# Performance work log

Measured on AMD Instinct MI355X. Metric: run time of the kernel, lower is better.

## Reference

```python
import jax, jax.numpy as jnp
import numpy as np

B, S, D_MODEL, N_HEAD, D_HEAD, GROUPS = 2, 1024, 768, 12, 64, 4
EPS = 1e-9
SCALE = 1.0 / np.sqrt(D_HEAD).astype(np.float32)


def grouped_proj(x, W, b=None):
    # grouped 1x1 Conv1d == block-diagonal linear. x: [B,S,D], W: [g, D/g, O/g]
    g = W.shape[0]
    b_, s_, d = x.shape
    y = jnp.einsum("bsgi,gio->bsgo", x.reshape(b_, s_, g, d // g), W).reshape(b_, s_, -1)
    return y if b is None else y + b


def rel_shift_gather(pos_attn, context_len, shift):
    # HF Funnel _relative_shift_gather
    b, n, s, m = pos_attn.shape
    pos_attn = pos_attn.reshape(b, n, m, s)[:, :, shift:, :]
    pos_attn = pos_attn.reshape(b, n, s, m - shift)[..., :context_len]
    return pos_attn


def setup_inputs() -> dict:
    key = jax.random.key(0)
    ks = jax.random.split(key, 16)
    dg = D_MODEL // GROUPS          # in-channels per group
    og = (N_HEAD * D_HEAD) // GROUPS  # out-channels per group
    std = 0.02
    return {
        "query": jax.random.normal(ks[0], (B, S, D_MODEL), jnp.float32),
        "position_embeds": jax.random.normal(ks[1], (2 * S - 1, D_MODEL), jnp.float32),
        "Wq": jax.random.normal(ks[2], (GROUPS, dg, og), jnp.float32) * std,
        "Wk": jax.random.normal(ks[3], (GROUPS, dg, og), jnp.float32) * std,
        "bk": jnp.zeros((N_HEAD * D_HEAD,), jnp.float32),
        "Wv": jax.random.normal(ks[4], (GROUPS, dg, dg), jnp.float32) * std,
        "bv": jnp.zeros((D_MODEL,), jnp.float32),
        "r_kernel": jax.random.normal(ks[5], (D_MODEL, N_HEAD, D_HEAD), jnp.float32) * std,
        "r_w_bias": jax.random.normal(ks[6], (N_HEAD, D_HEAD), jnp.float32) * std,
        "r_r_bias": jax.random.normal(ks[7], (N_HEAD, D_HEAD), jnp.float32) * std,
        "Wo": jax.random.normal(ks[8], (D_MODEL, D_MODEL), jnp.float32) * std,
        "bo": jnp.zeros((D_MODEL,), jnp.float32),
        "gamma": jnp.ones((D_MODEL,), jnp.float32),
        "beta": jnp.zeros((D_MODEL,), jnp.float32),
    }


def reference(query, position_embeds, Wq, Wk, bk, Wv, bv, r_kernel, r_w_bias,
              r_r_bias, Wo, bo, gamma, beta):
    b, s, _ = query.shape
    # q/k/v via grouped 1x1 convs
    q = grouped_proj(query, Wq).reshape(b, s, N_HEAD, D_HEAD) * SCALE
    k = grouped_proj(query, Wk, bk).reshape(b, s, N_HEAD, D_HEAD)
    v = grouped_proj(query, Wv, bv).reshape(b, s, N_HEAD, D_MODEL // N_HEAD)
    # content stream: (q + u) k^T
    content_score = jnp.einsum("bind,bjnd->bnij", q + r_w_bias * SCALE, k)
    # position stream: (q + v) r^T over 2S-1 relative positions, then rel-shift
    r_head = jnp.einsum("td,dnh->tnh", position_embeds, r_kernel)
    pos_score = jnp.einsum("bind,tnd->bnit", q + r_r_bias * SCALE, r_head)
    pos_score = rel_shift_gather(pos_score, s, shift=1)
    attn_prob = jax.nn.softmax(content_score + pos_score, axis=-1)
    attn_vec = jnp.einsum("bnij,bjnd->bind", attn_prob, v).reshape(b, s, D_MODEL)
    attn_out = attn_vec @ Wo + bo
    # residual + layer norm (eps=1e-9)
    h = query + attn_out
    mu = jnp.mean(h, axis=-1, keepdims=True)
    var = jnp.mean(jnp.square(h - mu), axis=-1, keepdims=True)
    return (h - mu) * jax.lax.rsqrt(var + EPS) * gamma + beta
```

## Files before the change

kernel.cpp:

```cpp
#include <hip/hip_runtime.h>
#include <stdint.h>

#define B_ 2
#define S_ 1024
#define D_ 768
#define H_ 12
#define DH 64
#define G_ 4
#define DG 192
#define T_ 2047
#define SCALEF 0.125f

typedef unsigned short u16;
typedef unsigned int u32;
typedef __attribute__((ext_vector_type(8))) short short8;
typedef __attribute__((ext_vector_type(4))) float floatx4;

__device__ __forceinline__ float uas(u32 x){ union { u32 i; float f; } v; v.i = x; return v.f; }
__device__ __forceinline__ float bf2f(u16 u){ return uas(((u32)u) << 16); }
__device__ __forceinline__ u16 f2bf(float f){
    union { float f; u32 i; } v; v.f = f;
    u32 x = v.i;
    u32 r = (x + 0x7fffu + ((x >> 16) & 1u)) >> 16;
    return (u16)r;
}

__global__ __launch_bounds__(256) void proj_kernel(
    const float* __restrict__ query,
    const float* __restrict__ Wq, const float* __restrict__ Wk, const float* __restrict__ Wv,
    const float* __restrict__ bk, const float* __restrict__ bv,
    u16* __restrict__ qq, u16* __restrict__ ko, u16* __restrict__ vt)
{
    __shared__ u16 As[64][40];
    __shared__ u16 Ws[3][64][38];
    int tid  = threadIdx.x;
    int wave = tid >> 6, lane = tid & 63;
    int qm   = lane & 15;
    int quad = lane >> 4;
    int k8   = quad * 8;
    int m0 = blockIdx.x * 64;
    int g  = blockIdx.y / 3;
    int n0 = (blockIdx.y % 3) * 64;

    const float* Wm[3] = { Wq, Wk, Wv };

    floatx4 acc[3][4];
    #pragma unroll
    for (int md = 0; md < 3; md++)
        #pragma unroll
        for (int bt = 0; bt < 4; bt++) acc[md][bt] = (floatx4){0.f,0.f,0.f,0.f};

    for (int kt = 0; kt < 6; kt++) {
        int k0 = kt * 32;
        #pragma unroll
        for (int p = 0; p < 8; p++) {
            int idx = p*256 + tid;
            int m = idx >> 5, k = idx & 31;
            As[m][k] = f2bf(query[(size_t)(m0 + m)*D_ + g*DG + k0 + k]);
        }
        #pragma unroll
        for (int md = 0; md < 3; md++) {
            const float* W = Wm[md] + (size_t)g*DG*DG;
            #pragma unroll
            for (int p = 0; p < 8; p++) {
                int k = p*4 + (tid >> 6);
                int n = tid & 63;
                Ws[md][n][k] = f2bf(W[(size_t)(k0 + k)*DG + n0 + n]);
            }
        }
        __syncthreads();
        short8 a = *(const short8*)&As[wave*16 + qm][k8];
        #pragma unroll
        for (int md = 0; md < 3; md++) {
            #pragma unroll
            for (int bt = 0; bt < 4; bt++) {
                short8 b = *(const short8*)&Ws[md][bt*16 + qm][k8];
                acc[md][bt] = __builtin_amdgcn_mfma_f32_16x16x32_bf16(a, b, acc[md][bt], 0,0,0);
            }
        }
        __syncthreads();
    }

    int rowbase = m0 + wave*16 + quad*4;
    int b  = rowbase >> 10;
    int s0 = rowbase & 1023;
    #pragma unroll
    for (int bt = 0; bt < 4; bt++) {
        int c = g*DG + n0 + bt*16 + qm;
        int n = c >> 6, d = c & 63;
        int bn = b*H_ + n;
        float bkv = bk[c], bvv = bv[c];
        #pragma unroll
        for (int gg = 0; gg < 4; gg++) {
            size_t o = ((size_t)bn*S_ + s0 + gg)*DH + d;
            qq[o] = f2bf(acc[0][bt][gg]*SCALEF);
            ko[o] = f2bf(acc[1][bt][gg] + bkv);
        }
        union { u16 h[4]; uint2 v; } vv;
        #pragma unroll
        for (int gg = 0; gg < 4; gg++) vv.h[gg] = f2bf(acc[2][bt][gg] + bvv);
        *(uint2*)(vt + ((size_t)bn*DH + d)*S_ + s0) = vv.v;
    }
}

template<int EPI, bool ABF16>
__global__ __launch_bounds__(256) void gemm_kernel(
    const void* __restrict__ A, const float* __restrict__ W,
    const float* __restrict__ bias, const float* __restrict__ resid,
    u16* __restrict__ outb, float* __restrict__ outf, int Mvalid)
{
    __shared__ u16 As[64][72];
    __shared__ u16 Ws[32][72];
    int tid  = threadIdx.x;
    int wave = tid >> 6, lane = tid & 63;
    int qm   = lane & 15;
    int quad = lane >> 4;
    int k8   = quad * 8;
    int m0 = blockIdx.x * 64;
    int n0 = blockIdx.y * 32;
    int wn = tid & 31, wk = tid >> 5;

    float4 af[4]; short8 ab[2]; float wf[8];
    floatx4 acc[2];
    acc[0] = (floatx4){0.f,0.f,0.f,0.f};
    acc[1] = (floatx4){0.f,0.f,0.f,0.f};

    if (ABF16) {
        #pragma unroll
        for (int p = 0; p < 2; p++) {
            int id = p*256 + tid; int m = id >> 3, kq = id & 7;
            ab[p] = *(const short8*)((const u16*)A + (size_t)(m0+m)*D_ + kq*8);
        }
    } else {
        #pragma unroll
        for (int p = 0; p < 4; p++) {
            int id = p*256 + tid; int m = id >> 4, kq = id & 15;
            int row = m0 + m; if (row >= Mvalid) row = Mvalid - 1;
            af[p] = *(const float4*)((const float*)A + (size_t)row*D_ + kq*4);
        }
    }
    #pragma unroll
    for (int p = 0; p < 8; p++) wf[p] = W[(size_t)(wk*8 + p)*D_ + n0 + wn];

    for (int kt = 0; kt < 12; kt++) {
        __syncthreads();
        if (ABF16) {
            #pragma unroll
            for (int p = 0; p < 2; p++) {
                int id = p*256 + tid; int m = id >> 3, kq = id & 7;
                *(short8*)&As[m][kq*8] = ab[p];
            }
        } else {
            #pragma unroll
            for (int p = 0; p < 4; p++) {
                int id = p*256 + tid; int m = id >> 4, kq = id & 15;
                union { u16 h[4]; uint2 v; } u;
                u.h[0] = f2bf(af[p].x); u.h[1] = f2bf(af[p].y);
                u.h[2] = f2bf(af[p].z); u.h[3] = f2bf(af[p].w);
                *(uint2*)&As[m][kq*4] = u.v;
            }
        }
        {
            union { u16 h[8]; short8 v; } w8;
            #pragma unroll
            for (int p = 0; p < 8; p++) w8.h[p] = f2bf(wf[p]);
            *(short8*)&Ws[wn][wk*8] = w8.v;
        }
        __syncthreads();
        if (kt < 11) {
            int k0 = (kt + 1) * 64;
            if (ABF16) {
                #pragma unroll
                for (int p = 0; p < 2; p++) {
                    int id = p*256 + tid; int m = id >> 3, kq = id & 7;
                    ab[p] = *(const short8*)((const u16*)A + (size_t)(m0+m)*D_ + k0 + kq*8);
                }
            } else {
                #pragma unroll
                for (int p = 0; p < 4; p++) {
                    int id = p*256 + tid; int m = id >> 4, kq = id & 15;
                    int row = m0 + m; if (row >= Mvalid) row = Mvalid - 1;
                    af[p] = *(const float4*)((const float*)A + (size_t)row*D_ + k0 + kq*4);
                }
            }
            #pragma unroll
            for (int p = 0; p < 8; p++) wf[p] = W[(size_t)(k0 + wk*8 + p)*D_ + n0 + wn];
        }
        #pragma unroll
        for (int ks = 0; ks < 2; ks++) {
            short8 a = *(const short8*)&As[wave*16 + qm][ks*32 + k8];
            #pragma unroll
            for (int bt = 0; bt < 2; bt++) {
                short8 b = *(const short8*)&Ws[bt*16 + qm][ks*32 + k8];
                acc[bt] = __builtin_amdgcn_mfma_f32_16x16x32_bf16(a, b, acc[bt], 0,0,0);
            }
        }
    }

    #pragma unroll
    for (int bt = 0; bt < 2; bt++) {
        int c = n0 + bt*16 + qm;
        #pragma unroll
        for (int g = 0; g < 4; g++) {
            int row = m0 + wave*16 + quad*4 + g;
            if (EPI == 0) {
                if (row < Mvalid)
                    outb[((size_t)(c >> 6)*T_ + row)*DH + (c & 63)] = f2bf(acc[bt][g]);
            } else {
                outf[(size_t)row*D_ + c] = acc[bt][g] + bias[c] + resid[(size_t)row*D_ + c];
            }
        }
    }
}

__global__ __launch_bounds__(256, 2) void attn_kernel(
    const u16* __restrict__ qq,
    const u16* __restrict__ kk, const u16* __restrict__ vt,
    const u16* __restrict__ R,
    const float* __restrict__ rwb, const float* __restrict__ rrb,
    u16* __restrict__ av)
{
    __shared__ char smem[64*1024];
    u16* SC  = (u16*)smem;
    u16* PSC = (u16*)(smem + 32768);
    int tid  = threadIdx.x;
    int wave = tid >> 6, lane = tid & 63;
    int qm   = lane & 15;
    int quad = lane >> 4;
    int k8   = quad * 8;
    int blkid = blockIdx.x;
    int xcd = blkid & 7;
    int sl  = blkid >> 3;
    int it  = sl & 63;
    int seg = sl >> 6;
    int bn  = xcd + 8*seg;
    int b = bn / H_, n = bn % H_;
    int i0 = it * 16;
    size_t hbase = (size_t)bn * S_ * DH;

    short8 qcf[2], qpf[2];
    #pragma unroll
    for (int s = 0; s < 2; s++) {
        const u16* qptr = qq + hbase + (size_t)(i0 + qm)*DH + s*32 + k8;
        const float* rwp = rwb + n*DH + s*32 + k8;
        const float* rrp = rrb + n*DH + s*32 + k8;
        #pragma unroll
        for (int j = 0; j < 8; j++) {
            float qv = bf2f(qptr[j]);
            qcf[s][j] = (short)f2bf(qv + rwp[j]*SCALEF);
            qpf[s][j] = (short)f2bf(qv + rrp[j]*SCALEF);
        }
    }

    {
        const u16* kbb = kk + hbase + (size_t)qm*DH + k8;
        short8 rb[8][2];
        #pragma unroll
        for (int t = 0; t < 8; t++) {
            const u16* kp = kbb + (size_t)((wave*16 + t)*16)*DH;
            rb[t][0] = *(const short8*)(kp);
            rb[t][1] = *(const short8*)(kp + 32);
        }
        #pragma unroll
        for (int t = 0; t < 16; t++) {
            short8 b0 = rb[t & 7][0], b1 = rb[t & 7][1];
            if (t < 8) {
                const u16* kp = kbb + (size_t)((wave*16 + t + 8)*16)*DH;
                rb[t & 7][0] = *(const short8*)(kp);
                rb[t & 7][1] = *(const short8*)(kp + 32);
            }
            floatx4 acc = {0.f,0.f,0.f,0.f};
            acc = __builtin_amdgcn_mfma_f32_16x16x32_bf16(qcf[0], b0, acc, 0,0,0);
            acc = __builtin_amdgcn_mfma_f32_16x16x32_bf16(qcf[1], b1, acc, 0,0,0);
            int j0 = (wave*16 + t) * 16;
            #pragma unroll
            for (int g = 0; g < 4; g++)
                SC[(quad*4 + g)*1024 + j0 + qm] = f2bf(acc[g]);
        }
    }

    int ubase = 1008 - i0;
    {
        const u16* rbb = R + (size_t)n*T_*DH + k8;
        short8 rb[8][2];
        int us[8];
        #pragma unroll
        for (int t = 0; t < 8; t++) {
            int m = t*4 + wave;
            int uu = ubase + m*16 + qm;
            int ur = (uu <= 2046) ? uu : 2046;
            us[t] = uu;
            const u16* rp = rbb + (size_t)ur*DH;
            rb[t][0] = *(const short8*)(rp);
            rb[t][1] = *(const short8*)(rp + 32);
        }
        #pragma unroll
        for (int t = 0; t < 16; t++) {
            short8 b0 = rb[t & 7][0], b1 = rb[t & 7][1];
            int uu = us[t & 7];
            if (t < 8) {
                int m2 = (t + 8)*4 + wave;
                int uu2 = ubase + m2*16 + qm;
                int ur2 = (uu2 <= 2046) ? uu2 : 2046;
                us[t & 7] = uu2;
                const u16* rp = rbb + (size_t)ur2*DH;
                rb[t & 7][0] = *(const short8*)(rp);
                rb[t & 7][1] = *(const short8*)(rp + 32);
            }
            floatx4 acc = {0.f,0.f,0.f,0.f};
            acc = __builtin_amdgcn_mfma_f32_16x16x32_bf16(qpf[0], b0, acc, 0,0,0);
            acc = __builtin_amdgcn_mfma_f32_16x16x32_bf16(qpf[1], b1, acc, 0,0,0);
            #pragma unroll
            for (int g = 0; g < 4; g++) {
                int row = quad*4 + g;
                int j = uu + i0 + row - 1024;
                if (j >= 0 && j < S_ && uu <= 2046)
                    PSC[row*1024 + j] = f2bf(acc[g]);
            }
        }
    }
    if (wave == 0) {
        int uu = ubase + 64*16 + qm;
        int ur = (uu <= 2046) ? uu : 2046;
        const u16* rp = R + ((size_t)n*T_ + ur)*DH + k8;
        short8 b0 = *(const short8*)(rp);
        short8 b1 = *(const short8*)(rp + 32);
        floatx4 acc = {0.f,0.f,0.f,0.f};
        acc = __builtin_amdgcn_mfma_f32_16x16x32_bf16(qpf[0], b0, acc, 0,0,0);
        acc = __builtin_amdgcn_mfma_f32_16x16x32_bf16(qpf[1], b1, acc, 0,0,0);
        #pragma unroll
        for (int g = 0; g < 4; g++) {
            int row = quad*4 + g;
            int j = uu + i0 + row - 1024;
            if (j >= 0 && j < S_ && uu <= 2046)
                PSC[row*1024 + j] = f2bf(acc[g]);
        }
    }
    if (i0 == 0 && tid == 0) {
        float sdot = 0.f;
        const u16* r0p = R + (size_t)n*T_*DH;
        const u16* q1p = qq + hbase + DH;
        for (int d = 0; d < DH; d++)
            sdot += (bf2f(q1p[d]) + rrb[n*DH + d]*SCALEF) * bf2f(r0p[d]);
        PSC[1023] = f2bf(sdot);
    }
    __syncthreads();

    for (int rr = 0; rr < 4; rr++) {
        int r = wave*4 + rr;
        short8 c0 = *(const short8*)(SC  + r*1024 + lane*16);
        short8 c1 = *(const short8*)(SC  + r*1024 + lane*16 + 8);
        short8 p0 = *(const short8*)(PSC + r*1024 + lane*16);
        short8 p1 = *(const short8*)(PSC + r*1024 + lane*16 + 8);
        float p[16];
        float mx = -1e30f;
        #pragma unroll
        for (int q = 0; q < 8; q++) {
            p[q]   = bf2f((u16)c0[q]) + bf2f((u16)p0[q]);
            p[q+8] = bf2f((u16)c1[q]) + bf2f((u16)p1[q]);
        }
        #pragma unroll
        for (int q = 0; q < 16; q++) mx = fmaxf(mx, p[q]);
        #pragma unroll
        for (int off = 32; off; off >>= 1) mx = fmaxf(mx, __shfl_xor(mx, off));
        float ssum = 0.f;
        #pragma unroll
        for (int q = 0; q < 16; q++) { p[q] = __expf(p[q] - mx); ssum += p[q]; }
        #pragma unroll
        for (int off = 32; off; off >>= 1) ssum += __shfl_xor(ssum, off);
        float inv = 1.0f / ssum;
        int swz = r & 7;
        union { u16 h[8]; short8 v; } w0, w1;
        #pragma unroll
        for (int q = 0; q < 8; q++) {
            w0.h[q] = f2bf(p[q]*inv);
            w1.h[q] = f2bf(p[q+8]*inv);
        }
        *(short8*)(SC + r*1024 + (((2*lane)   ^ swz) << 3)) = w0.v;
        *(short8*)(SC + r*1024 + (((2*lane+1) ^ swz) << 3)) = w1.v;
    }

    int d0 = wave*16;
    const u16* vbase = vt + ((size_t)bn*DH + d0 + qm)*S_;
    short8 vb[8];
    #pragma unroll
    for (int t = 0; t < 8; t++) vb[t] = *(const short8*)(vbase + t*32 + k8);
    __syncthreads();

    floatx4 o[4];
    #pragma unroll
    for (int t = 0; t < 4; t++) o[t] = (floatx4){0.f,0.f,0.f,0.f};
    int aswz = qm & 7;
    #pragma unroll
    for (int kt = 0; kt < 32; kt++) {
        short8 bfr = vb[kt & 7];
        if (kt < 24) vb[kt & 7] = *(const short8*)(vbase + (kt + 8)*32 + k8);
        int chunk = (kt*4 + quad) ^ aswz;
        short8 a = *(const short8*)(SC + qm*1024 + (chunk << 3));
        o[kt & 3] = __builtin_amdgcn_mfma_f32_16x16x32_bf16(a, bfr, o[kt & 3], 0,0,0);
    }
    floatx4 os = (o[0] + o[1]) + (o[2] + o[3]);
    #pragma unroll
    for (int g = 0; g < 4; g++) {
        int row = quad*4 + g;
        av[((size_t)(b*S_) + i0 + row)*D_ + n*DH + d0 + qm] = f2bf(os[g]);
    }
}

__global__ __launch_bounds__(256) void ln_kernel(
    const float* __restrict__ gamma, const float* __restrict__ beta,
    float* out)
{
    __shared__ float hb[8][D_];
    int tid = threadIdx.x;
    int rowg0 = blockIdx.x * 8;
    #pragma unroll
    for (int p = 0; p < 6; p++) {
        int id = p*256 + tid;
        int r = id / 192, e4 = id % 192;
        *(float4*)&hb[r][e4*4] = *(const float4*)&out[(size_t)(rowg0 + r)*D_ + e4*4];
    }
    __syncthreads();
    int wave = tid >> 6, lane = tid & 63;
    for (int rr = 0; rr < 2; rr++) {
        int r = wave*2 + rr;
        float s = 0.f;
        #pragma unroll
        for (int kq = 0; kq < 12; kq++) s += hb[r][lane + kq*64];
        #pragma unroll
        for (int off = 32; off; off >>= 1) s += __shfl_xor(s, off);
        float mu = s * (1.0f/768.0f);
        float vsum = 0.f;
        #pragma unroll
        for (int kq = 0; kq < 12; kq++) { float d = hb[r][lane + kq*64] - mu; vsum += d*d; }
        #pragma unroll
        for (int off = 32; off; off >>= 1) vsum += __shfl_xor(vsum, off);
        float rstd = rsqrtf(vsum * (1.0f/768.0f) + 1e-9f);
        #pragma unroll
        for (int kq = 0; kq < 3; kq++) {
            int c4 = lane + kq*64;
            float4 g4 = *(const float4*)&gamma[c4*4];
            float4 b4 = *(const float4*)&beta[c4*4];
            float4 h4 = *(const float4*)&hb[r][c4*4];
            float4 o4;
            o4.x = (h4.x - mu)*rstd*g4.x + b4.x;
            o4.y = (h4.y - mu)*rstd*g4.y + b4.y;
            o4.z = (h4.z - mu)*rstd*g4.z + b4.z;
            o4.w = (h4.w - mu)*rstd*g4.w + b4.w;
            *(float4*)&out[(size_t)(rowg0 + r)*D_ + c4*4] = o4;
        }
    }
}

extern "C" void kernel_launch(void* const* d_in, const int* in_sizes, int n_in,
                              void* d_out, int out_size, void* d_ws, size_t ws_size,
                              hipStream_t stream) {
    const float* query = (const float*)d_in[0];
    const float* pe    = (const float*)d_in[1];
    const float* Wq    = (const float*)d_in[2];
    const float* Wk    = (const float*)d_in[3];
    const float* bk    = (const float*)d_in[4];
    const float* Wv    = (const float*)d_in[5];
    const float* bv    = (const float*)d_in[6];
    const float* rk    = (const float*)d_in[7];
    const float* rwb   = (const float*)d_in[8];
    const float* rrb   = (const float*)d_in[9];
    const float* Wo    = (const float*)d_in[10];
    const float* bo    = (const float*)d_in[11];
    const float* gamma = (const float*)d_in[12];
    const float* beta  = (const float*)d_in[13];
    float* out = (float*)d_out;

    u16* ws = (u16*)d_ws;
    const size_t SEG = (size_t)B_*H_*S_*DH;
    u16* qq = ws;
    u16* kk = qq + SEG;
    u16* vt = kk + SEG;
    u16* R  = vt + SEG;
    u16* av = R + SEG;

    proj_kernel<<<dim3(32,12), 256, 0, stream>>>(query, Wq, Wk, Wv, bk, bv, qq, kk, vt);
    gemm_kernel<0,false><<<dim3(32,24), 256, 0, stream>>>(pe, rk, nullptr, nullptr, R, nullptr, T_);
    attn_kernel<<<1536, 256, 0, stream>>>(qq, kk, vt, R, rwb, rrb, av);
    gemm_kernel<1,true><<<dim3(32,24), 256, 0, stream>>>(av, Wo, bo, query, nullptr, out, B_*S_);
    ln_kernel<<<256, 256, 0, stream>>>(gamma, beta, out);
}
```

Baseline: 207.2 us.

## Pre-convert inputs to bf16 and pre-transpose weights for vectorized GEMM loads

Adds a conversion kernel that casts query and position embeddings to bf16, and a transpose kernel that writes bf16 transposed copies of all weight matrices. The projection and GEMM kernels then load 16-byte bf16 vectors into a k-major shared layout, with register prefetch, instead of doing scalar fp32 loads and converting in-loop. The GEMM N tile is widened from 32 to 64. This removes uncoalesced scalar weight reads and repeated conversions, at the cost of two extra launches and extra traffic. It also reuses the output buffer as scratch and aliases av with qb.

```diff
diff --git a/kernel.cpp b/kernel.cpp
--- a/kernel.cpp
+++ b/kernel.cpp
@@ -25,24 +25,102 @@
     return (u16)r;
 }
 
+__global__ __launch_bounds__(256) void conv_kernel(
+    const float* __restrict__ query, const float* __restrict__ pe,
+    u16* __restrict__ qb, u16* __restrict__ peb)
+{
+    int t = blockIdx.x*256 + threadIdx.x;
+    #pragma unroll
+    for (int p = 0; p < 2; p++) {
+        int u = t + p*196608;
+        float4 v = *(const float4*)(query + (size_t)u*4);
+        union { u16 h[4]; uint2 w; } o;
+        o.h[0]=f2bf(v.x); o.h[1]=f2bf(v.y); o.h[2]=f2bf(v.z); o.h[3]=f2bf(v.w);
+        *(uint2*)(qb + (size_t)u*4) = o.w;
+    }
+    #pragma unroll
+    for (int p = 0; p < 2; p++) {
+        int u = t + p*196608;
+        if (u < 393024) {
+            float4 v = *(const float4*)(pe + (size_t)u*4);
+            union { u16 h[4]; uint2 w; } o;
+            o.h[0]=f2bf(v.x); o.h[1]=f2bf(v.y); o.h[2]=f2bf(v.z); o.h[3]=f2bf(v.w);
+            *(uint2*)(peb + (size_t)u*4) = o.w;
+        }
+    }
+}
+
+__global__ __launch_bounds__(256) void trans_kernel(
+    const float* __restrict__ rk, const float* __restrict__ Wo,
+    const float* __restrict__ Wq, const float* __restrict__ Wk, const float* __restrict__ Wv,
+    u16* __restrict__ rkT, u16* __restrict__ WoT,
+    u16* __restrict__ WqT, u16* __restrict__ WkT, u16* __restrict__ WvT)
+{
+    __shared__ u16 T[64][72];
+    int tid = threadIdx.x;
+    int z = blockIdx.z;
+    int tx = blockIdx.x, ty = blockIdx.y;
+    const float* src; u16* dst; int KN;
+    if (z == 0)      { src = rk; dst = rkT; KN = 768; }
+    else if (z == 1) { src = Wo; dst = WoT; KN = 768; }
+    else {
+        if (tx >= 3) return;
+        const float* W3[3] = {Wq, Wk, Wv};
+        u16* D3[3] = {WqT, WkT, WvT};
+        int gg = ty / 3; ty = ty % 3;
+        src = W3[z-2] + (size_t)gg*DG*DG;
+        dst = D3[z-2] + (size_t)gg*DG*DG;
+        KN = 192;
+    }
+    int k0 = tx*64, n0 = ty*64;
+    int r = tid >> 2, c0 = (tid & 3) * 16;
+    #pragma unroll
+    for (int q = 0; q < 4; q++) {
+        float4 v = *(const float4*)(src + (size_t)(k0+r)*KN + n0 + c0 + q*4);
+        T[c0+q*4+0][r] = f2bf(v.x);
+        T[c0+q*4+1][r] = f2bf(v.y);
+        T[c0+q*4+2][r] = f2bf(v.z);
+        T[c0+q*4+3][r] = f2bf(v.w);
+    }
+    __syncthreads();
+    int n = tid >> 2, kc0 = (tid & 3) * 16;
+    uint4 w0 = *(uint4*)&T[n][kc0];
+    uint4 w1 = *(uint4*)&T[n][kc0 + 8];
+    *(uint4*)(dst + (size_t)(n0+n)*KN + k0 + kc0)     = w0;
+    *(uint4*)(dst + (size_t)(n0+n)*KN + k0 + kc0 + 8) = w1;
+}
+
 __global__ __launch_bounds__(256) void proj_kernel(
-    const float* __restrict__ query,
-    const float* __restrict__ Wq, const float* __restrict__ Wk, const float* __restrict__ Wv,
+    const u16* __restrict__ qb,
+    const u16* __restrict__ WqT, const u16* __restrict__ WkT, const u16* __restrict__ WvT,
     const float* __restrict__ bk, const float* __restrict__ bv,
     u16* __restrict__ qq, u16* __restrict__ ko, u16* __restrict__ vt)
 {
-    __shared__ u16 As[64][40];
-    __shared__ u16 Ws[3][64][38];
+    __shared__ u16 As[8][64][8];
+    __shared__ u16 Ws[3][8][64][8];
     int tid  = threadIdx.x;
     int wave = tid >> 6, lane = tid & 63;
     int qm   = lane & 15;
     int quad = lane >> 4;
-    int k8   = quad * 8;
     int m0 = blockIdx.x * 64;
     int g  = blockIdx.y / 3;
     int n0 = (blockIdx.y % 3) * 64;
-
-    const float* Wm[3] = { Wq, Wk, Wv };
+    int mA = tid & 63, ko0 = tid >> 6;
+
+    const u16* Abase = qb + (size_t)(m0 + mA)*D_ + g*DG;
+    const u16* Wb[3] = {
+        WqT + (size_t)g*DG*DG + (size_t)(n0 + mA)*DG,
+        WkT + (size_t)g*DG*DG + (size_t)(n0 + mA)*DG,
+        WvT + (size_t)g*DG*DG + (size_t)(n0 + mA)*DG };
+
+    short8 ra[2], rw[3][2];
+    ra[0] = *(const short8*)(Abase + ko0*8);
+    ra[1] = *(const short8*)(Abase + (ko0+4)*8);
+    #pragma unroll
+    for (int md = 0; md < 3; md++) {
+        rw[md][0] = *(const short8*)(Wb[md] + ko0*8);
+        rw[md][1] = *(const short8*)(Wb[md] + (ko0+4)*8);
+    }
 
     floatx4 acc[3][4];
     #pragma unroll
@@ -50,35 +128,38 @@
         #pragma unroll
         for (int bt = 0; bt < 4; bt++) acc[md][bt] = (floatx4){0.f,0.f,0.f,0.f};
 
-    for (int kt = 0; kt < 6; kt++) {
-        int k0 = kt * 32;
-        #pragma unroll
-        for (int p = 0; p < 8; p++) {
-            int idx = p*256 + tid;
-            int m = idx >> 5, k = idx & 31;
-            As[m][k] = f2bf(query[(size_t)(m0 + m)*D_ + g*DG + k0 + k]);
-        }
+    for (int kt = 0; kt < 3; kt++) {
+        __syncthreads();
+        *(short8*)&As[ko0][mA][0]   = ra[0];
+        *(short8*)&As[ko0+4][mA][0] = ra[1];
         #pragma unroll
         for (int md = 0; md < 3; md++) {
-            const float* W = Wm[md] + (size_t)g*DG*DG;
+            *(short8*)&Ws[md][ko0][mA][0]   = rw[md][0];
+            *(short8*)&Ws[md][ko0+4][mA][0] = rw[md][1];
+        }
+        __syncthreads();
+        if (kt < 2) {
+            int k0 = (kt + 1) * 64;
+            ra[0] = *(const short8*)(Abase + k0 + ko0*8);
+            ra[1] = *(const short8*)(Abase + k0 + (ko0+4)*8);
             #pragma unroll
-            for (int p = 0; p < 8; p++) {
-                int k = p*4 + (tid >> 6);
-                int n = tid & 63;
-                Ws[md][n][k] = f2bf(W[(size_t)(k0 + k)*DG + n0 + n]);
-            }
-        }
-        __syncthreads();
-        short8 a = *(const short8*)&As[wave*16 + qm][k8];
-        #pragma unroll
-        for (int md = 0; md < 3; md++) {
+            for (int md = 0; md < 3; md++) {
+                rw[md][0] = *(const short8*)(Wb[md] + k0 + ko0*8);
+                rw[md][1] = *(const short8*)(Wb[md] + k0 + (ko0+4)*8);
+            }
+        }
+        #pragma unroll
+        for (int ks = 0; ks < 2; ks++) {
+            short8 a = *(const short8*)&As[ks*4 + quad][wave*16 + qm][0];
             #pragma unroll
-            for (int bt = 0; bt < 4; bt++) {
-                short8 b = *(const short8*)&Ws[md][bt*16 + qm][k8];
-                acc[md][bt] = __builtin_amdgcn_mfma_f32_16x16x32_bf16(a, b, acc[md][bt], 0,0,0);
-            }
-        }
-        __syncthreads();
+            for (int md = 0; md < 3; md++) {
+                #pragma unroll
+                for (int bt = 0; bt < 4; bt++) {
+                    short8 b = *(const short8*)&Ws[md][ks*4 + quad][bt*16 + qm][0];
+                    acc[md][bt] = __builtin_amdgcn_mfma_f32_16x16x32_bf16(a, b, acc[md][bt], 0,0,0);
+                }
+            }
+        }
     }
 
     int rowbase = m0 + wave*16 + quad*4;
@@ -103,102 +184,63 @@
     }
 }
 
-template<int EPI, bool ABF16>
+template<int EPI>
 __global__ __launch_bounds__(256) void gemm_kernel(
-    const void* __restrict__ A, const float* __restrict__ W,
+    const u16* __restrict__ A, const u16* __restrict__ WT,
     const float* __restrict__ bias, const float* __restrict__ resid,
     u16* __restrict__ outb, float* __restrict__ outf, int Mvalid)
 {
-    __shared__ u16 As[64][72];
-    __shared__ u16 Ws[32][72];
+    __shared__ u16 As[8][64][8];
+    __shared__ u16 Ws[8][64][8];
     int tid  = threadIdx.x;
     int wave = tid >> 6, lane = tid & 63;
     int qm   = lane & 15;
     int quad = lane >> 4;
-    int k8   = quad * 8;
     int m0 = blockIdx.x * 64;
-    int n0 = blockIdx.y * 32;
-    int wn = tid & 31, wk = tid >> 5;
-
-    float4 af[4]; short8 ab[2]; float wf[8];
-    floatx4 acc[2];
-    acc[0] = (floatx4){0.f,0.f,0.f,0.f};
-    acc[1] = (floatx4){0.f,0.f,0.f,0.f};
-
-    if (ABF16) {
-        #pragma unroll
-        for (int p = 0; p < 2; p++) {
-            int id = p*256 + tid; int m = id >> 3, kq = id & 7;
-            ab[p] = *(const short8*)((const u16*)A + (size_t)(m0+m)*D_ + kq*8);
-        }
-    } else {
-        #pragma unroll
-        for (int p = 0; p < 4; p++) {
-            int id = p*256 + tid; int m = id >> 4, kq = id & 15;
-            int row = m0 + m; if (row >= Mvalid) row = Mvalid - 1;
-            af[p] = *(const float4*)((const float*)A + (size_t)row*D_ + kq*4);
-        }
-    }
-    #pragma unroll
-    for (int p = 0; p < 8; p++) wf[p] = W[(size_t)(wk*8 + p)*D_ + n0 + wn];
+    int n0 = blockIdx.y * 64;
+    int mA = tid & 63, ko0 = tid >> 6;
+
+    int rowA = m0 + mA; if (rowA >= Mvalid) rowA = Mvalid - 1;
+    const u16* Abase = A  + (size_t)rowA*D_;
+    const u16* Wbase = WT + (size_t)(n0 + mA)*D_;
+
+    short8 ra[2], rw[2];
+    ra[0] = *(const short8*)(Abase + ko0*8);
+    ra[1] = *(const short8*)(Abase + (ko0+4)*8);
+    rw[0] = *(const short8*)(Wbase + ko0*8);
+    rw[1] = *(const short8*)(Wbase + (ko0+4)*8);
+
+    floatx4 acc[4];
+    #pragma unroll
+    for (int t = 0; t < 4; t++) acc[t] = (floatx4){0.f,0.f,0.f,0.f};
 
     for (int kt = 0; kt < 12; kt++) {
         __syncthreads();
-        if (ABF16) {
-            #pragma unroll
-            for (int p = 0; p < 2; p++) {
-                int id = p*256 + tid; int m = id >> 3, kq = id & 7;
-                *(short8*)&As[m][kq*8] = ab[p];
-            }
-        } else {
-            #pragma unroll
-            for (int p = 0; p < 4; p++) {
-                int id = p*256 + tid; int m = id >> 4, kq = id & 15;
-                union { u16 h[4]; uint2 v; } u;
-                u.h[0] = f2bf(af[p].x); u.h[1] = f2bf(af[p].y);
-                u.h[2] = f2bf(af[p].z); u.h[3] = f2bf(af[p].w);
-                *(uint2*)&As[m][kq*4] = u.v;
-            }
-        }
-        {
-            union { u16 h[8]; short8 v; } w8;
-            #pragma unroll
-            for (int p = 0; p < 8; p++) w8.h[p] = f2bf(wf[p]);
-            *(short8*)&Ws[wn][wk*8] = w8.v;
-        }
+        *(short8*)&As[ko0][mA][0]   = ra[0];
+        *(short8*)&As[ko0+4][mA][0] = ra[1];
+        *(short8*)&Ws[ko0][mA][0]   = rw[0];
+        *(short8*)&Ws[ko0+4][mA][0] = rw[1];
         __syncthreads();
         if (kt < 11) {
             int k0 = (kt + 1) * 64;
-            if (ABF16) {
-                #pragma unroll
-                for (int p = 0; p < 2; p++) {
-                    int id = p*256 + tid; int m = id >> 3, kq = id & 7;
-                    ab[p] = *(const short8*)((const u16*)A + (size_t)(m0+m)*D_ + k0 + kq*8);
-                }
-            } else {
-                #pragma unroll
-                for (int p = 0; p < 4; p++) {
-                    int id = p*256 + tid; int m = id >> 4, kq = id & 15;
-                    int row = m0 + m; if (row >= Mvalid) row = Mvalid - 1;
-                    af[p] = *(const float4*)((const float*)A + (size_t)row*D_ + k0 + kq*4);
-                }
-            }
+            ra[0] = *(const short8*)(Abase + k0 + ko0*8);
+            ra[1] = *(const short8*)(Abase + k0 + (ko0+4)*8);
+            rw[0] = *(const short8*)(Wbase + k0 + ko0*8);
+            rw[1] = *(const short8*)(Wbase + k0 + (ko0+4)*8);
+        }
+        #pragma unroll
+        for (int ks = 0; ks < 2; ks++) {
+            short8 a = *(const short8*)&As[ks*4 + quad][wave*16 + qm][0];
             #pragma unroll
-            for (int p = 0; p < 8; p++) wf[p] = W[(size_t)(k0 + wk*8 + p)*D_ + n0 + wn];
-        }
-        #pragma unroll
-        for (int ks = 0; ks < 2; ks++) {
-            short8 a = *(const short8*)&As[wave*16 + qm][ks*32 + k8];
-            #pragma unroll
-            for (int bt = 0; bt < 2; bt++) {
-                short8 b = *(const short8*)&Ws[bt*16 + qm][ks*32 + k8];
+            for (int bt = 0; bt < 4; bt++) {
+                short8 b = *(const short8*)&Ws[ks*4 + quad][bt*16 + qm][0];
                 acc[bt] = __builtin_amdgcn_mfma_f32_16x16x32_bf16(a, b, acc[bt], 0,0,0);
             }
         }
     }
 
     #pragma unroll
-    for (int bt = 0; bt < 2; bt++) {
+    for (int bt = 0; bt < 4; bt++) {
         int c = n0 + bt*16 + qm;
         #pragma unroll
         for (int g = 0; g < 4; g++) {
@@ -473,15 +515,25 @@
 
     u16* ws = (u16*)d_ws;
     const size_t SEG = (size_t)B_*H_*S_*DH;
-    u16* qq = ws;
-    u16* kk = qq + SEG;
-    u16* vt = kk + SEG;
-    u16* R  = vt + SEG;
-    u16* av = R + SEG;
-
-    proj_kernel<<<dim3(32,12), 256, 0, stream>>>(query, Wq, Wk, Wv, bk, bv, qq, kk, vt);
-    gemm_kernel<0,false><<<dim3(32,24), 256, 0, stream>>>(pe, rk, nullptr, nullptr, R, nullptr, T_);
+    u16* qq  = ws;
+    u16* kk  = qq + SEG;
+    u16* vt  = kk + SEG;
+    u16* R   = vt + SEG;
+    u16* qb  = R  + SEG;
+    u16* WoT = qb + SEG;
+    u16* WqT = WoT + (size_t)D_*D_;
+    u16* WkT = WqT + (size_t)G_*DG*DG;
+    u16* WvT = WkT + (size_t)G_*DG*DG;
+    u16* av  = qb;
+
+    u16* peb = (u16*)d_out;
+    u16* rkT = peb + SEG;
+
+    conv_kernel<<<768, 256, 0, stream>>>(query, pe, qb, peb);
+    trans_kernel<<<dim3(12,12,5), 256, 0, stream>>>(rk, Wo, Wq, Wk, Wv, rkT, WoT, WqT, WkT, WvT);
+    proj_kernel<<<dim3(32,12), 256, 0, stream>>>(qb, WqT, WkT, WvT, bk, bv, qq, kk, vt);
+    gemm_kernel<0><<<dim3(32,12), 256, 0, stream>>>(peb, rkT, nullptr, nullptr, R, nullptr, T_);
     attn_kernel<<<1536, 256, 0, stream>>>(qq, kk, vt, R, rwb, rrb, av);
-    gemm_kernel<1,true><<<dim3(32,24), 256, 0, stream>>>(av, Wo, bo, query, nullptr, out, B_*S_);
+    gemm_kernel<1><<<dim3(32,12), 256, 0, stream>>>(av, WoT, bo, query, nullptr, out, B_*S_);
     ln_kernel<<<256, 256, 0, stream>>>(gamma, beta, out);
 }
```

Measured after the change: 214.7 us. +3.6%, slower.

## Merge QKV and position projections into one launch; stage full-K weights in LDS

Applied to the files above, without the earlier changes.

The grouped QKV projection and the relative-position projection now run as a single launch, with block index selecting the branch. This removes one kernel launch and lets both halves share the GPU. Both this kernel and the output GEMM now load the entire K-extent of the weight tile into shared memory once and keep A operands in registers loaded straight from global, replacing the per-k-tile LDS double-stage loop and its barriers. The trade-offs are larger LDS footprints (~49KB), which may lower occupancy, and strided scalar weight loads.

```diff
diff --git a/kernel.cpp b/kernel.cpp
--- a/kernel.cpp
+++ b/kernel.cpp
@@ -24,176 +24,191 @@
     u32 r = (x + 0x7fffu + ((x >> 16) & 1u)) >> 16;
     return (u16)r;
 }
-
-__global__ __launch_bounds__(256) void proj_kernel(
+__device__ __forceinline__ short8 cvt8(float4 x, float4 y){
+    union { u16 h[8]; short8 v; } u;
+    u.h[0]=f2bf(x.x); u.h[1]=f2bf(x.y); u.h[2]=f2bf(x.z); u.h[3]=f2bf(x.w);
+    u.h[4]=f2bf(y.x); u.h[5]=f2bf(y.y); u.h[6]=f2bf(y.z); u.h[7]=f2bf(y.w);
+    return u.v;
+}
+
+__global__ __launch_bounds__(256) void pre_kernel(
     const float* __restrict__ query,
     const float* __restrict__ Wq, const float* __restrict__ Wk, const float* __restrict__ Wv,
     const float* __restrict__ bk, const float* __restrict__ bv,
-    u16* __restrict__ qq, u16* __restrict__ ko, u16* __restrict__ vt)
+    u16* __restrict__ qq, u16* __restrict__ ko, u16* __restrict__ vt,
+    const float* __restrict__ pe, const float* __restrict__ rk,
+    u16* __restrict__ R)
 {
-    __shared__ u16 As[64][40];
-    __shared__ u16 Ws[3][64][38];
+    __shared__ __align__(16) char sm[49664];
     int tid  = threadIdx.x;
     int wave = tid >> 6, lane = tid & 63;
     int qm   = lane & 15;
     int quad = lane >> 4;
-    int k8   = quad * 8;
-    int m0 = blockIdx.x * 64;
-    int g  = blockIdx.y / 3;
-    int n0 = (blockIdx.y % 3) * 64;
-
-    const float* Wm[3] = { Wq, Wk, Wv };
-
-    floatx4 acc[3][4];
-    #pragma unroll
-    for (int md = 0; md < 3; md++)
-        #pragma unroll
-        for (int bt = 0; bt < 4; bt++) acc[md][bt] = (floatx4){0.f,0.f,0.f,0.f};
-
-    for (int kt = 0; kt < 6; kt++) {
-        int k0 = kt * 32;
-        #pragma unroll
-        for (int p = 0; p < 8; p++) {
-            int idx = p*256 + tid;
-            int m = idx >> 5, k = idx & 31;
-            As[m][k] = f2bf(query[(size_t)(m0 + m)*D_ + g*DG + k0 + k]);
+    int id = blockIdx.x;
+    int sn = tid & 31, sk = tid >> 5;
+
+    if (id < 768) {
+        typedef u16 (*W3T)[32][200];
+        W3T Ws = (W3T)sm;
+        int m0 = (id & 31) * 64;
+        int gy = id >> 5;
+        int g  = gy / 6;
+        int n0 = (gy % 6) * 32;
+        const float* Wm[3] = { Wq, Wk, Wv };
+
+        int row = m0 + wave*16 + qm;
+        const float* Ab = query + (size_t)row*D_ + g*DG;
+        float4 fx[6], fy[6];
+        #pragma unroll
+        for (int kc = 0; kc < 6; kc++) {
+            fx[kc] = *(const float4*)(Ab + kc*32 + quad*8);
+            fy[kc] = *(const float4*)(Ab + kc*32 + quad*8 + 4);
         }
         #pragma unroll
         for (int md = 0; md < 3; md++) {
-            const float* W = Wm[md] + (size_t)g*DG*DG;
-            #pragma unroll
-            for (int p = 0; p < 8; p++) {
-                int k = p*4 + (tid >> 6);
-                int n = tid & 63;
-                Ws[md][n][k] = f2bf(W[(size_t)(k0 + k)*DG + n0 + n]);
-            }
+            const float* W = Wm[md] + (size_t)g*DG*DG + n0 + sn;
+            #pragma unroll
+            for (int k = 0; k < 24; k++)
+                Ws[md][sn][sk + k*8] = f2bf(W[(size_t)(sk + k*8)*DG]);
         }
         __syncthreads();
-        short8 a = *(const short8*)&As[wave*16 + qm][k8];
-        #pragma unroll
-        for (int md = 0; md < 3; md++) {
-            #pragma unroll
-            for (int bt = 0; bt < 4; bt++) {
-                short8 b = *(const short8*)&Ws[md][bt*16 + qm][k8];
-                acc[md][bt] = __builtin_amdgcn_mfma_f32_16x16x32_bf16(a, b, acc[md][bt], 0,0,0);
-            }
+
+        short8 af[6];
+        #pragma unroll
+        for (int kc = 0; kc < 6; kc++) af[kc] = cvt8(fx[kc], fy[kc]);
+
+        floatx4 acc[3][2];
+        #pragma unroll
+        for (int md = 0; md < 3; md++) { acc[md][0] = (floatx4){0,0,0,0}; acc[md][1] = (floatx4){0,0,0,0}; }
+        #pragma unroll
+        for (int kc = 0; kc < 6; kc++) {
+            short8 a = af[kc];
+            #pragma unroll
+            for (int md = 0; md < 3; md++) {
+                #pragma unroll
+                for (int bt = 0; bt < 2; bt++) {
+                    short8 b = *(const short8*)&Ws[md][bt*16 + qm][kc*32 + quad*8];
+                    acc[md][bt] = __builtin_amdgcn_mfma_f32_16x16x32_bf16(a, b, acc[md][bt], 0,0,0);
+                }
+            }
+        }
+
+        int rowbase = m0 + wave*16 + quad*4;
+        int b  = rowbase >> 10;
+        int s0 = rowbase & 1023;
+        #pragma unroll
+        for (int bt = 0; bt < 2; bt++) {
+            int c = g*DG + n0 + bt*16 + qm;
+            int n = c >> 6, d = c & 63;
+            int bn = b*H_ + n;
+            float bkv = bk[c], bvv = bv[c];
+            #pragma unroll
+            for (int gg = 0; gg < 4; gg++) {
+                size_t o = ((size_t)bn*S_ + s0 + gg)*DH + d;
+                qq[o] = f2bf(acc[0][bt][gg]*SCALEF);
+                ko[o] = f2bf(acc[1][bt][gg] + bkv);
+            }
+            union { u16 h[4]; uint2 v; } vv;
+            #pragma unroll
+            for (int gg = 0; gg < 4; gg++) vv.h[gg] = f2bf(acc[2][bt][gg] + bvv);
+            *(uint2*)(vt + ((size_t)bn*DH + d)*S_ + s0) = vv.v;
+        }
+    } else {
+        typedef u16 (*WsT)[776];
+        WsT Ws = (WsT)sm;
+        int id2 = id - 768;
+        int m0 = (id2 & 31) * 64;
+        int n0 = (id2 >> 5) * 32;
+
+        int row = m0 + wave*16 + qm;
+        int rowc = (row <= 2046) ? row : 2046;
+        const float* Ab = pe + (size_t)rowc*D_;
+
+        float4 fr[4][2];
+        #pragma unroll
+        for (int t = 0; t < 4; t++) {
+            fr[t][0] = *(const float4*)(Ab + t*32 + quad*8);
+            fr[t][1] = *(const float4*)(Ab + t*32 + quad*8 + 4);
+        }
+        {
+            const float* W = rk + n0 + sn;
+            #pragma unroll
+            for (int k = 0; k < 96; k++)
+                Ws[sn][sk + k*8] = f2bf(W[(size_t)(sk + k*8)*D_]);
         }
         __syncthreads();
-    }
-
-    int rowbase = m0 + wave*16 + quad*4;
-    int b  = rowbase >> 10;
-    int s0 = rowbase & 1023;
-    #pragma unroll
-    for (int bt = 0; bt < 4; bt++) {
-        int c = g*DG + n0 + bt*16 + qm;
-        int n = c >> 6, d = c & 63;
-        int bn = b*H_ + n;
-        float bkv = bk[c], bvv = bv[c];
-        #pragma unroll
-        for (int gg = 0; gg < 4; gg++) {
-            size_t o = ((size_t)bn*S_ + s0 + gg)*DH + d;
-            qq[o] = f2bf(acc[0][bt][gg]*SCALEF);
-            ko[o] = f2bf(acc[1][bt][gg] + bkv);
-        }
-        union { u16 h[4]; uint2 v; } vv;
-        #pragma unroll
-        for (int gg = 0; gg < 4; gg++) vv.h[gg] = f2bf(acc[2][bt][gg] + bvv);
-        *(uint2*)(vt + ((size_t)bn*DH + d)*S_ + s0) = vv.v;
-    }
-}
-
-template<int EPI, bool ABF16>
-__global__ __launch_bounds__(256) void gemm_kernel(
-    const void* __restrict__ A, const float* __restrict__ W,
+
+        floatx4 acc[2];
+        acc[0] = (floatx4){0,0,0,0};
+        acc[1] = (floatx4){0,0,0,0};
+        #pragma unroll
+        for (int kc = 0; kc < 24; kc++) {
+            float4 x = fr[kc & 3][0], y = fr[kc & 3][1];
+            if (kc < 20) {
+                fr[kc & 3][0] = *(const float4*)(Ab + (kc+4)*32 + quad*8);
+                fr[kc & 3][1] = *(const float4*)(Ab + (kc+4)*32 + quad*8 + 4);
+            }
+            short8 a = cvt8(x, y);
+            #pragma unroll
+            for (int bt = 0; bt < 2; bt++) {
+                short8 b = *(const short8*)&Ws[bt*16 + qm][kc*32 + quad*8];
+                acc[bt] = __builtin_amdgcn_mfma_f32_16x16x32_bf16(a, b, acc[bt], 0,0,0);
+            }
+        }
+
+        #pragma unroll
+        for (int bt = 0; bt < 2; bt++) {
+            int c = n0 + bt*16 + qm;
+            #pragma unroll
+            for (int g = 0; g < 4; g++) {
+                int r2 = m0 + wave*16 + quad*4 + g;
+                if (r2 < T_)
+                    R[((size_t)(c >> 6)*T_ + r2)*DH + (c & 63)] = f2bf(acc[bt][g]);
+            }
+        }
+    }
+}
+
+__global__ __launch_bounds__(256) void gemm_out_kernel(
+    const u16* __restrict__ A, const float* __restrict__ W,
     const float* __restrict__ bias, const float* __restrict__ resid,
-    u16* __restrict__ outb, float* __restrict__ outf, int Mvalid)
+    float* __restrict__ outf)
 {
-    __shared__ u16 As[64][72];
-    __shared__ u16 Ws[32][72];
+    __shared__ __align__(16) u16 Ws[32][776];
     int tid  = threadIdx.x;
     int wave = tid >> 6, lane = tid & 63;
     int qm   = lane & 15;
     int quad = lane >> 4;
-    int k8   = quad * 8;
-    int m0 = blockIdx.x * 64;
-    int n0 = blockIdx.y * 32;
-    int wn = tid & 31, wk = tid >> 5;
-
-    float4 af[4]; short8 ab[2]; float wf[8];
+    int id = blockIdx.x;
+    int m0 = (id & 31) * 64;
+    int n0 = (id >> 5) * 32;
+    int sn = tid & 31, sk = tid >> 5;
+
+    int row = m0 + wave*16 + qm;
+    const u16* Ab = A + (size_t)row*D_;
+
+    short8 ar[8];
+    #pragma unroll
+    for (int t = 0; t < 8; t++) ar[t] = *(const short8*)(Ab + t*32 + quad*8);
+    {
+        const float* Wb = W + n0 + sn;
+        #pragma unroll
+        for (int k = 0; k < 96; k++)
+            Ws[sn][sk + k*8] = f2bf(Wb[(size_t)(sk + k*8)*D_]);
+    }
+    __syncthreads();
+
     floatx4 acc[2];
-    acc[0] = (floatx4){0.f,0.f,0.f,0.f};
-    acc[1] = (floatx4){0.f,0.f,0.f,0.f};
-
-    if (ABF16) {
-        #pragma unroll
-        for (int p = 0; p < 2; p++) {
-            int id = p*256 + tid; int m = id >> 3, kq = id & 7;
-            ab[p] = *(const short8*)((const u16*)A + (size_t)(m0+m)*D_ + kq*8);
-        }
-    } else {
-        #pragma unroll
-        for (int p = 0; p < 4; p++) {
-            int id = p*256 + tid; int m = id >> 4, kq = id & 15;
-            int row = m0 + m; if (row >= Mvalid) row = Mvalid - 1;
-            af[p] = *(const float4*)((const float*)A + (size_t)row*D_ + kq*4);
-        }
-    }
-    #pragma unroll
-    for (int p = 0; p < 8; p++) wf[p] = W[(size_t)(wk*8 + p)*D_ + n0 + wn];
-
-    for (int kt = 0; kt < 12; kt++) {
-        __syncthreads();
-        if (ABF16) {
-            #pragma unroll
-            for (int p = 0; p < 2; p++) {
-                int id = p*256 + tid; int m = id >> 3, kq = id & 7;
-                *(short8*)&As[m][kq*8] = ab[p];
-            }
-        } else {
-            #pragma unroll
-            for (int p = 0; p < 4; p++) {
-                int id = p*256 + tid; int m = id >> 4, kq = id & 15;
-                union { u16 h[4]; uint2 v; } u;
-                u.h[0] = f2bf(af[p].x); u.h[1] = f2bf(af[p].y);
-                u.h[2] = f2bf(af[p].z); u.h[3] = f2bf(af[p].w);
-                *(uint2*)&As[m][kq*4] = u.v;
-            }
-        }
-        {
-            union { u16 h[8]; short8 v; } w8;
-            #pragma unroll
-            for (int p = 0; p < 8; p++) w8.h[p] = f2bf(wf[p]);
-            *(short8*)&Ws[wn][wk*8] = w8.v;
-        }
-        __syncthreads();
-        if (kt < 11) {
-            int k0 = (kt + 1) * 64;
-            if (ABF16) {
-                #pragma unroll
-                for (int p = 0; p < 2; p++) {
-                    int id = p*256 + tid; int m = id >> 3, kq = id & 7;
-                    ab[p] = *(const short8*)((const u16*)A + (size_t)(m0+m)*D_ + k0 + kq*8);
-                }
-            } else {
-                #pragma unroll
-                for (int p = 0; p < 4; p++) {
-                    int id = p*256 + tid; int m = id >> 4, kq = id & 15;
-                    int row = m0 + m; if (row >= Mvalid) row = Mvalid - 1;
-                    af[p] = *(const float4*)((const float*)A + (size_t)row*D_ + k0 + kq*4);
-                }
-            }
-            #pragma unroll
-            for (int p = 0; p < 8; p++) wf[p] = W[(size_t)(k0 + wk*8 + p)*D_ + n0 + wn];
-        }
-        #pragma unroll
-        for (int ks = 0; ks < 2; ks++) {
-            short8 a = *(const short8*)&As[wave*16 + qm][ks*32 + k8];
-            #pragma unroll
-            for (int bt = 0; bt < 2; bt++) {
-                short8 b = *(const short8*)&Ws[bt*16 + qm][ks*32 + k8];
-                acc[bt] = __builtin_amdgcn_mfma_f32_16x16x32_bf16(a, b, acc[bt], 0,0,0);
-            }
+    acc[0] = (floatx4){0,0,0,0};
+    acc[1] = (floatx4){0,0,0,0};
+    #pragma unroll
+    for (int kc = 0; kc < 24; kc++) {
+        short8 a = ar[kc & 7];
+        if (kc < 16) ar[kc & 7] = *(const short8*)(Ab + (kc+8)*32 + quad*8);
+        #pragma unroll
+        for (int bt = 0; bt < 2; bt++) {
+            short8 b = *(const short8*)&Ws[bt*16 + qm][kc*32 + quad*8];
+            acc[bt] = __builtin_amdgcn_mfma_f32_16x16x32_bf16(a, b, acc[bt], 0,0,0);
         }
     }
 
@@ -202,13 +217,8 @@
         int c = n0 + bt*16 + qm;
         #pragma unroll
         for (int g = 0; g < 4; g++) {
-            int row = m0 + wave*16 + quad*4 + g;
-            if (EPI == 0) {
-                if (row < Mvalid)
-                    outb[((size_t)(c >> 6)*T_ + row)*DH + (c & 63)] = f2bf(acc[bt][g]);
-            } else {
-                outf[(size_t)row*D_ + c] = acc[bt][g] + bias[c] + resid[(size_t)row*D_ + c];
-            }
+            int r2 = m0 + wave*16 + quad*4 + g;
+            outf[(size_t)r2*D_ + c] = acc[bt][g] + bias[c] + resid[(size_t)r2*D_ + c];
         }
     }
 }
@@ -479,9 +489,8 @@
     u16* R  = vt + SEG;
     u16* av = R + SEG;
 
-    proj_kernel<<<dim3(32,12), 256, 0, stream>>>(query, Wq, Wk, Wv, bk, bv, qq, kk, vt);
-    gemm_kernel<0,false><<<dim3(32,24), 256, 0, stream>>>(pe, rk, nullptr, nullptr, R, nullptr, T_);
+    pre_kernel<<<1536, 256, 0, stream>>>(query, Wq, Wk, Wv, bk, bv, qq, kk, vt, pe, rk, R);
     attn_kernel<<<1536, 256, 0, stream>>>(qq, kk, vt, R, rwb, rrb, av);
-    gemm_kernel<1,true><<<dim3(32,24), 256, 0, stream>>>(av, Wo, bo, query, nullptr, out, B_*S_);
+    gemm_out_kernel<<<768, 256, 0, stream>>>(av, Wo, bo, query, out);
     ln_kernel<<<256, 256, 0, stream>>>(gamma, beta, out);
 }
```

Result: slower. 212.3 us (+2.5%).
